# Optimization experiments

Measured on AMD Instinct MI355X. Metric: run time of the kernel, lower is better.

Reference implementation:

```python
import jax, jax.numpy as jnp
import numpy as np

N_HEAD = 8  # config.n_head

def _ln(x, g, b):
    # eqx.nn.LayerNorm, eps=1e-5
    m = x.mean(-1, keepdims=True)
    v = ((x - m) ** 2).mean(-1, keepdims=True)
    return (x - m) / jnp.sqrt(v + 1e-5) * g + b

def _lin(x, w, b):
    # eqx.nn.Linear: weight [out, in]
    return x @ w.T + b

def _heads(t):
    B, T, C = t.shape
    return t.reshape(B, T, N_HEAD, C // N_HEAD).transpose(0, 2, 1, 3)  # [B,H,T,d]

def _merge(t):
    B, H, T, d = t.shape
    return t.transpose(0, 2, 1, 3).reshape(B, T, H * d)

def setup_inputs() -> dict:
    key = jax.random.key(0)
    B, T1, T2, C, INNER, NIN = 4, 4096, 4096, 512, 2048, 2
    ks = jax.random.split(key, 16)
    w = lambda k, *s: 0.02 * jax.random.normal(k, s, dtype=jnp.float32)
    return {
        'x': jax.random.normal(ks[0], (B, T1, C), dtype=jnp.float32),
        'ys': jax.random.normal(ks[1], (NIN, B, T2, C), dtype=jnp.float32),
        'ln1_g': jnp.ones((C,)), 'ln1_b': jnp.zeros((C,)),
        'ln2_g': jnp.ones((NIN, C)), 'ln2_b': jnp.zeros((NIN, C)),
        'ln3_g': jnp.ones((C,)), 'ln3_b': jnp.zeros((C,)),
        'ln4_g': jnp.ones((C,)), 'ln4_b': jnp.zeros((C,)),
        'ln5_g': jnp.ones((C,)), 'ln5_b': jnp.zeros((C,)),
        'ca_wq': w(ks[2], C, C), 'ca_bq': jnp.zeros((C,)),
        'ca_wk': w(ks[3], NIN, C, C), 'ca_bk': jnp.zeros((NIN, C)),
        'ca_wv': w(ks[4], NIN, C, C), 'ca_bv': jnp.zeros((NIN, C)),
        'ca_wo': w(ks[5], C, C), 'ca_bo': jnp.zeros((C,)),
        'sa_wq': w(ks[6], C, C), 'sa_bq': jnp.zeros((C,)),
        'sa_wk': w(ks[7], C, C), 'sa_bk': jnp.zeros((C,)),
        'sa_wv': w(ks[8], C, C), 'sa_bv': jnp.zeros((C,)),
        'sa_wo': w(ks[9], C, C), 'sa_bo': jnp.zeros((C,)),
        'ffn1_w1': w(ks[10], INNER, C), 'ffn1_b1': jnp.zeros((INNER,)),
        'ffn1_w2': w(ks[11], C, INNER), 'ffn1_b2': jnp.zeros((C,)),
        'ffn2_w1': w(ks[12], INNER, C), 'ffn2_b1': jnp.zeros((INNER,)),
        'ffn2_w2': w(ks[13], C, INNER), 'ffn2_b2': jnp.zeros((C,)),
    }

def reference(x, ys, ln1_g, ln1_b, ln2_g, ln2_b, ln3_g, ln3_b, ln4_g, ln4_b, ln5_g, ln5_b,
              ca_wq, ca_bq, ca_wk, ca_bk, ca_wv, ca_bv, ca_wo, ca_bo,
              sa_wq, sa_bq, sa_wk, sa_bk, sa_wv, sa_bv, sa_wo, sa_bo,
              ffn1_w1, ffn1_b1, ffn1_w2, ffn1_b2, ffn2_w1, ffn2_b1, ffn2_w2, ffn2_b2):
    n_inputs = ys.shape[0]
    # ---- linear cross attention ----
    xn = _ln(x, ln1_g, ln1_b)
    q = jax.nn.softmax(_heads(_lin(xn, ca_wq, ca_bq)), axis=-1)  # [B,H,T1,d]
    out = q
    for i in range(n_inputs):  # small fixed branch count
        yn = _ln(ys[i], ln2_g[i], ln2_b[i])
        k = jax.nn.softmax(_heads(_lin(yn, ca_wk[i], ca_bk[i])), axis=-1)  # [B,H,T2,d]
        v = _heads(_lin(yn, ca_wv[i], ca_bv[i]))
        k_sum = k.sum(axis=-2, keepdims=True)                       # [B,H,1,d]
        D_inv = 1.0 / ((q * k_sum).sum(axis=-1, keepdims=True) + 1e-8)
        ctx = jnp.einsum('bhnd,bhnv->bhdv', k, v)                   # [B,H,d,d]
        out = out + jnp.einsum('bhqd,bhdv->bhqv', q, ctx) * D_inv
    x = x + _lin(_merge(out), ca_wo, ca_bo)
    # ---- FFN 1 ----
    xn = _ln(x, ln3_g, ln3_b)
    x = x + _lin(jax.nn.gelu(_lin(xn, ffn1_w1, ffn1_b1)), ffn1_w2, ffn1_b2)
    # ---- linear self attention (attn_type='l1') ----
    xn = _ln(x, ln4_g, ln4_b)
    q = jax.nn.softmax(_heads(_lin(xn, sa_wq, sa_bq)), axis=-1)
    k = jax.nn.softmax(_heads(_lin(xn, sa_wk, sa_bk)), axis=-1)
    v = _heads(_lin(xn, sa_wv, sa_bv))
    k_sum = k.sum(axis=-2, keepdims=True)
    D_inv = 1.0 / (q * k_sum).sum(axis=-1, keepdims=True)  # no eps in 'l1' branch
    ctx = jnp.einsum('bhnd,bhnv->bhdv', k, v)
    sa = jnp.einsum('bhqd,bhdv->bhqv', q, ctx) * D_inv + q
    x = x + _lin(_merge(sa), sa_wo, sa_bo)
    # ---- FFN 2 ----
    xn = _ln(x, ln5_g, ln5_b)
    x = x + _lin(jax.nn.gelu(_lin(xn, ffn2_w1, ffn2_b1)), ffn2_w2, ffn2_b2)
    return x
```

## Files before the change

kernel.cpp:

```cpp
#include <hip/hip_runtime.h>
#include <hip/hip_bf16.h>
#include <math.h>
#include <stdint.h>

typedef unsigned short u16;
typedef __attribute__((ext_vector_type(8))) short bh8;
typedef __attribute__((ext_vector_type(4))) float fx4;

#define DEV static __device__ __forceinline__

DEV float bf2f(u16 u){ union{unsigned u; float f;} v; v.u = ((unsigned)u)<<16; return v.f; }
DEV u16 f2bf(float f){ union{float f; unsigned u;} v; v.f = f;
  return (u16)((v.u + 0x7fffu + ((v.u>>16)&1u))>>16); }

DEV void async16(const u16* g, u16* l){
  __builtin_amdgcn_global_load_lds((__attribute__((address_space(1))) void*)(uintptr_t)g,
                                   (__attribute__((address_space(3))) void*)l, 16, 0, 0);
}

DEV float gelu_fast(float x){
  float u = 0.7978845608f*(x + 0.044715f*x*x*x);
  float e = __expf(-2.f*fabsf(u));
  float t = __fdividef(1.f - e, 1.f + e);
  t = copysignf(t, u);
  return 0.5f*x*(1.f + t);
}

struct WDesc { const float* src[14]; int off[14]; };
__global__ __launch_bounds__(256) void convw_kernel(WDesc d, u16* __restrict__ dst){
  int i = blockIdx.x*256 + threadIdx.x;
  int s = 0;
  #pragma unroll
  for(int j=1;j<14;j++) if(i >= d.off[j]) s = j;
  dst[i] = f2bf(d.src[s][i - d.off[s]]);
}

DEV float wsum64(float s){
  s += __shfl_xor(s,1,64);  s += __shfl_xor(s,2,64);  s += __shfl_xor(s,4,64);
  s += __shfl_xor(s,8,64);  s += __shfl_xor(s,16,64); s += __shfl_xor(s,32,64);
  return s;
}
__global__ __launch_bounds__(256) void ln_kernel(const float* __restrict__ x,
    const float* __restrict__ g, const float* __restrict__ bta, u16* __restrict__ out){
  int row  = blockIdx.x*4 + (threadIdx.x>>6);
  int lane = threadIdx.x & 63;
  const float4* xr = (const float4*)(x + (size_t)row*512) + lane*2;
  float4 a = xr[0], c = xr[1];
  float s = a.x+a.y+a.z+a.w + c.x+c.y+c.z+c.w;
  float mean = wsum64(s) * (1.f/512.f);
  float d0=a.x-mean,d1=a.y-mean,d2=a.z-mean,d3=a.w-mean;
  float d4=c.x-mean,d5=c.y-mean,d6=c.z-mean,d7=c.w-mean;
  float sv = d0*d0+d1*d1+d2*d2+d3*d3+d4*d4+d5*d5+d6*d6+d7*d7;
  float rstd = rsqrtf(wsum64(sv)*(1.f/512.f) + 1e-5f);
  const float4* gr = (const float4*)g   + lane*2;
  const float4* br = (const float4*)bta + lane*2;
  float4 g0=gr[0], g1=gr[1], b0=br[0], b1=br[1];
  bh8 o;
  o[0]=(short)f2bf(d0*rstd*g0.x+b0.x); o[1]=(short)f2bf(d1*rstd*g0.y+b0.y);
  o[2]=(short)f2bf(d2*rstd*g0.z+b0.z); o[3]=(short)f2bf(d3*rstd*g0.w+b0.w);
  o[4]=(short)f2bf(d4*rstd*g1.x+b1.x); o[5]=(short)f2bf(d5*rstd*g1.y+b1.y);
  o[6]=(short)f2bf(d6*rstd*g1.z+b1.z); o[7]=(short)f2bf(d7*rstd*g1.w+b1.w);
  *(bh8*)(out + (size_t)row*512 + lane*8) = o;
}

#define GEMM_KLOOP(Ab, Wb, K)                                                        \
  const int srow = w*32 + (lane>>2);                                                 \
  const int scol = (((lane&3) ^ ((srow>>1)&3)) * 8);                                 \
  const int rsw  = ((l15>>1)&3) ^ quad;                \
  for(int k0=0;k0<K;k0+=32){                                                         \
    __syncthreads();                                                                 \
    async16(Ab + (size_t)srow*K      + k0 + scol, &lsA[(w*32   )*32]);               \
    async16(Ab + (size_t)(srow+16)*K + k0 + scol, &lsA[(w*32+16)*32]);               \
    async16(Wb + (size_t)srow*K      + k0 + scol, &lsB[(w*32   )*32]);               \
    async16(Wb + (size_t)(srow+16)*K + k0 + scol, &lsB[(w*32+16)*32]);               \
    __syncthreads();                                                                 \
    bh8 af[4], bfx[4];                                                               \
    _Pragma("unroll")                                                                \
    for(int t=0;t<4;t++){                                                            \
      af[t]  = *(const bh8*)&lsA[(wm*64+t*16+l15)*32 + rsw*8];                       \
      bfx[t] = *(const bh8*)&lsB[(wn*64+t*16+l15)*32 + rsw*8];                       \
    }                                                                                \
    _Pragma("unroll")                                                                \
    for(int mt=0;mt<4;mt++)                                                          \
      _Pragma("unroll")                                                              \
      for(int nt=0;nt<4;nt++)                                                        \
        acc[mt][nt] = __builtin_amdgcn_mfma_f32_16x16x32_bf16(af[mt], bfx[nt], acc[mt][nt], 0,0,0); \
  }

struct SubD { const float* bias; u16* out; float* ksum; int mode; };
struct Subs3 { SubD s[3]; };
__global__ __launch_bounds__(256) void gemm_qkv(const u16* __restrict__ A,
    const u16* __restrict__ W, Subs3 subs, int K){
  __shared__ __align__(16) u16 lsA[128*32];
  __shared__ __align__(16) u16 lsB[128*32];
  const int tid = threadIdx.x, lane = tid&63, w = tid>>6;
  const int quad = lane>>4, l15 = lane&15;
  const int bn = blockIdx.x, bm = blockIdx.y;
  const int wm = w&1, wn = w>>1;
  fx4 acc[4][4];
  #pragma unroll
  for(int i=0;i<4;i++)
    #pragma unroll
    for(int j=0;j<4;j++) acc[i][j] = (fx4){0.f,0.f,0.f,0.f};
  const u16* Ab = A + (size_t)bm*128*K;
  const u16* Wb = W + (size_t)bn*128*K;
  GEMM_KLOOP(Ab, Wb, K)
  const SubD sub = subs.s[bn>>2];
  const int colw = (bn&3)*128 + wn*64;
  float bcol[4];
  #pragma unroll
  for(int nt=0;nt<4;nt++) bcol[nt] = sub.bias[colw + nt*16 + l15];

  if(sub.mode==1){
    float ksacc[4] = {0.f,0.f,0.f,0.f};
    #pragma unroll
    for(int mt=0;mt<4;mt++)
      #pragma unroll
      for(int r=0;r<4;r++){
        float v0=acc[mt][0][r]+bcol[0], v1=acc[mt][1][r]+bcol[1];
        float v2=acc[mt][2][r]+bcol[2], v3=acc[mt][3][r]+bcol[3];
        float mx = fmaxf(fmaxf(v0,v1),fmaxf(v2,v3));
        mx = fmaxf(mx,__shfl_xor(mx,1,64)); mx = fmaxf(mx,__shfl_xor(mx,2,64));
        mx = fmaxf(mx,__shfl_xor(mx,4,64)); mx = fmaxf(mx,__shfl_xor(mx,8,64));
        float e0=__expf(v0-mx), e1=__expf(v1-mx), e2=__expf(v2-mx), e3=__expf(v3-mx);
        float s = e0+e1+e2+e3;
        s += __shfl_xor(s,1,64); s += __shfl_xor(s,2,64);
        s += __shfl_xor(s,4,64); s += __shfl_xor(s,8,64);
        float inv = __fdividef(1.f, s);
        e0*=inv; e1*=inv; e2*=inv; e3*=inv;
        ksacc[0]+=e0; ksacc[1]+=e1; ksacc[2]+=e2; ksacc[3]+=e3;
        int row = bm*128 + wm*64 + mt*16 + quad*4 + r;
        size_t rb = (size_t)row*512;
        sub.out[rb+colw+ 0+l15]=f2bf(e0); sub.out[rb+colw+16+l15]=f2bf(e1);
        sub.out[rb+colw+32+l15]=f2bf(e2); sub.out[rb+colw+48+l15]=f2bf(e3);
      }
    if(sub.ksum){
      int b = bm>>5;
      #pragma unroll
      for(int nt=0;nt<4;nt++){
        float s = ksacc[nt];
        s += __shfl_xor(s,16,64); s += __shfl_xor(s,32,64);
        if(quad==0) atomicAdd(&sub.ksum[b*512 + colw + nt*16 + l15], s);
      }
    }
  } else {
    #pragma unroll
    for(int mt=0;mt<4;mt++)
      #pragma unroll
      for(int r=0;r<4;r++){
        int row = bm*128 + wm*64 + mt*16 + quad*4 + r;
        size_t rb = (size_t)row*512;
        #pragma unroll
        for(int nt=0;nt<4;nt++)
          sub.out[rb + colw + nt*16 + l15] = f2bf(acc[mt][nt][r] + bcol[nt]);
      }
  }
}

template<int EPI>
__global__ __launch_bounds__(256) void gemm_bt(const u16* __restrict__ A,
    const u16* __restrict__ W, const float* __restrict__ bias,
    const float* __restrict__ res, void* __restrict__ out, int N, int K){
  __shared__ __align__(16) u16 lsA[128*32];
  __shared__ __align__(16) u16 lsB[128*32];
  const int tid = threadIdx.x, lane = tid&63, w = tid>>6;
  const int quad = lane>>4, l15 = lane&15;
  const int bn = blockIdx.x, bm = blockIdx.y;
  const int wm = w&1, wn = w>>1;
  fx4 acc[4][4];
  #pragma unroll
  for(int i=0;i<4;i++)
    #pragma unroll
    for(int j=0;j<4;j++) acc[i][j] = (fx4){0.f,0.f,0.f,0.f};
  const u16* Ab = A + (size_t)bm*128*K;
  const u16* Wb = W + (size_t)bn*128*K;
  GEMM_KLOOP(Ab, Wb, K)
  const int colbase = bn*128 + wn*64;
  float bcol[4];
  #pragma unroll
  for(int nt=0;nt<4;nt++) bcol[nt] = bias[colbase + nt*16 + l15];

  if(EPI==3){
    float* of = (float*)out;
    #pragma unroll
    for(int mt=0;mt<4;mt++)
      #pragma unroll
      for(int r=0;r<4;r++){
        int row = bm*128 + wm*64 + mt*16 + quad*4 + r;
        size_t rb = (size_t)row*N;
        #pragma unroll
        for(int nt=0;nt<4;nt++){
          int col = colbase + nt*16 + l15;
          of[rb+col] = res[rb+col] + acc[mt][nt][r] + bcol[nt];
        }
      }
  } else {
    u16* ob = (u16*)out;
    #pragma unroll
    for(int mt=0;mt<4;mt++)
      #pragma unroll
      for(int r=0;r<4;r++){
        int row = bm*128 + wm*64 + mt*16 + quad*4 + r;
        size_t rb = (size_t)row*N;
        #pragma unroll
        for(int nt=0;nt<4;nt++)
          ob[rb + colbase + nt*16 + l15] = f2bf(gelu_fast(acc[mt][nt][r] + bcol[nt]));
      }
  }
}

__global__ __launch_bounds__(256) void ctx_kernel(const u16* __restrict__ kb,
    const u16* __restrict__ vb, float* __restrict__ ctx){
  __shared__ __align__(16) u16 lk[64*72];
  __shared__ __align__(16) u16 lv[64*72];
  const int tid=threadIdx.x, lane=tid&63, w=tid>>6, quad=lane>>4, l15=lane&15;
  const int bh = blockIdx.x, h = bh&7;
  const size_t rowbase = ((size_t)(bh>>3))*4096 + (size_t)blockIdx.y*512;
  const int mt0=(w&1)*32, nt0=(w>>1)*32;
  fx4 acc[2][2];
  #pragma unroll
  for(int i=0;i<2;i++)
    #pragma unroll
    for(int j=0;j<2;j++) acc[i][j] = (fx4){0.f,0.f,0.f,0.f};
  const int tl = tid>>2, part = tid&3;
  for(int it=0; it<8; it++){
    __syncthreads();
    {
      size_t gro = (rowbase + it*64 + tl)*512 + h*64 + part*16;
      bh8 k0 = *(const bh8*)(kb + gro); bh8 k1 = *(const bh8*)(kb + gro + 8);
      bh8 v0 = *(const bh8*)(vb + gro); bh8 v1 = *(const bh8*)(vb + gro + 8);
      #pragma unroll
      for(int j=0;j<8;j++){
        lk[(part*16+j  )*72 + tl] = (u16)k0[j];
        lk[(part*16+8+j)*72 + tl] = (u16)k1[j];
        lv[(part*16+j  )*72 + tl] = (u16)v0[j];
        lv[(part*16+8+j)*72 + tl] = (u16)v1[j];
      }
    }
    __syncthreads();
    #pragma unroll
    for(int ks=0;ks<2;ks++){
      bh8 a0 = *(const bh8*)&lk[(mt0    +l15)*72 + ks*32 + quad*8];
      bh8 a1 = *(const bh8*)&lk[(mt0+16 +l15)*72 + ks*32 + quad*8];
      bh8 b0 = *(const bh8*)&lv[(nt0    +l15)*72 + ks*32 + quad*8];
      bh8 b1 = *(const bh8*)&lv[(nt0+16 +l15)*72 + ks*32 + quad*8];
      acc[0][0] = __builtin_amdgcn_mfma_f32_16x16x32_bf16(a0,b0,acc[0][0],0,0,0);
      acc[0][1] = __builtin_amdgcn_mfma_f32_16x16x32_bf16(a0,b1,acc[0][1],0,0,0);
      acc[1][0] = __builtin_amdgcn_mfma_f32_16x16x32_bf16(a1,b0,acc[1][0],0,0,0);
      acc[1][1] = __builtin_amdgcn_mfma_f32_16x16x32_bf16(a1,b1,acc[1][1],0,0,0);
    }
  }
  float* cb = ctx + (size_t)bh*4096;
  #pragma unroll
  for(int mi=0;mi<2;mi++)
    #pragma unroll
    for(int ni=0;ni<2;ni++)
      #pragma unroll
      for(int r=0;r<4;r++){
        int d1 = mt0 + mi*16 + quad*4 + r;
        int d2 = nt0 + ni*16 + l15;
        atomicAdd(&cb[d1*64 + d2], acc[mi][ni][r]);
      }
}

__global__ __launch_bounds__(256) void dinv_kernel(const u16* __restrict__ q,
    const float* __restrict__ ksum, float* __restrict__ dinv, int n_in, float eps){
  int gidx = blockIdx.x*256 + threadIdx.x;
  int token = gidx>>3, h = gidx&7, b = token>>12;
  const u16* qr = q + (size_t)token*512 + h*64;
  float qv[64];
  #pragma unroll
  for(int d=0;d<64;d++) qv[d] = bf2f(qr[d]);
  for(int i=0;i<n_in;i++){
    const float* ks = ksum + i*2048 + b*512 + h*64;
    float s = 0.f;
    #pragma unroll
    for(int d=0;d<64;d++) s += qv[d]*ks[d];
    dinv[(size_t)i*131072 + gidx] = __fdividef(1.f, s + eps);
  }
}

template<int NIN>
__global__ __launch_bounds__(256) void apply_kernel(const u16* __restrict__ q,
    const float* __restrict__ ctx, const float* __restrict__ dinv, u16* __restrict__ out){
  __shared__ __align__(16) u16 lctx[(NIN+1)*64*72];
  const int tid=threadIdx.x, lane=tid&63, w=tid>>6, quad=lane>>4, l15=lane&15;
  const int bh = blockIdx.x, b=bh>>3, h=bh&7;
  {
    int base = tid*16;
    int d1 = base>>6, d2b = base&63;
    #pragma unroll
    for(int s=0;s<=NIN;s++){
      u16* dst = &lctx[s*64*72];
      if(s<NIN){
        const float* sp = ctx + ((size_t)s*32 + bh)*4096 + base;
        #pragma unroll
        for(int j=0;j<16;j++) dst[(d2b+j)*72 + d1] = f2bf(sp[j]);
      } else {
        #pragma unroll
        for(int j=0;j<16;j++) dst[(d2b+j)*72 + d1] = ((d2b+j)==d1) ? (u16)0x3f80 : (u16)0;
      }
    }
  }
  __syncthreads();
  bh8 bfr[NIN+1][4][2];
  #pragma unroll
  for(int s=0;s<=NIN;s++)
    #pragma unroll
    for(int nt=0;nt<4;nt++)
      #pragma unroll
      for(int ks=0;ks<2;ks++)
        bfr[s][nt][ks] = *(const bh8*)&lctx[s*64*72 + (nt*16+l15)*72 + ks*32 + quad*8];
  const size_t tb0 = (size_t)b*4096 + (size_t)blockIdx.y*256 + w*64;
  for(int g=0;g<4;g++){
    size_t tb = tb0 + g*16;
    const u16* qr = q + (tb + l15)*512 + h*64;
    bh8 a0 = *(const bh8*)(qr + quad*8);
    bh8 a1 = *(const bh8*)(qr + 32 + quad*8);
    fx4 outv[4];
    #pragma unroll
    for(int nt=0;nt<4;nt++) outv[nt] = (fx4){0.f,0.f,0.f,0.f};
    #pragma unroll
    for(int s=0;s<=NIN;s++){
      fx4 c[4];
      #pragma unroll
      for(int nt=0;nt<4;nt++){
        c[nt] = (fx4){0.f,0.f,0.f,0.f};
        c[nt] = __builtin_amdgcn_mfma_f32_16x16x32_bf16(a0, bfr[s][nt][0], c[nt], 0,0,0);
        c[nt] = __builtin_amdgcn_mfma_f32_16x16x32_bf16(a1, bfr[s][nt][1], c[nt], 0,0,0);
      }
      float dv[4];
      #pragma unroll
      for(int r=0;r<4;r++)
        dv[r] = (s==NIN) ? 1.f : dinv[(size_t)s*131072 + (tb+quad*4+r)*8 + h];
      #pragma unroll
      for(int nt=0;nt<4;nt++)
        #pragma unroll
        for(int r=0;r<4;r++) outv[nt][r] += c[nt][r]*dv[r];
    }
    #pragma unroll
    for(int nt=0;nt<4;nt++)
      #pragma unroll
      for(int r=0;r<4;r++)
        out[(tb+quad*4+r)*512 + h*64 + nt*16 + l15] = f2bf(outv[nt][r]);
  }
}

extern "C" void kernel_launch(void* const* d_in, const int* in_sizes, int n_in,
                              void* d_out, int out_size, void* d_ws, size_t ws_size,
                              hipStream_t stream){
  const float* x_in =(const float*)d_in[0];
  const float* ys   =(const float*)d_in[1];
  const float* ln1g =(const float*)d_in[2],  *ln1b=(const float*)d_in[3];
  const float* ln2g =(const float*)d_in[4],  *ln2b=(const float*)d_in[5];
  const float* ln3g =(const float*)d_in[6],  *ln3b=(const float*)d_in[7];
  const float* ln4g =(const float*)d_in[8],  *ln4b=(const float*)d_in[9];
  const float* ln5g =(const float*)d_in[10], *ln5b=(const float*)d_in[11];
  const float* ca_wq=(const float*)d_in[12], *ca_bq=(const float*)d_in[13];
  const float* ca_wk=(const float*)d_in[14], *ca_bk=(const float*)d_in[15];
  const float* ca_wv=(const float*)d_in[16], *ca_bv=(const float*)d_in[17];
  const float* ca_wo=(const float*)d_in[18], *ca_bo=(const float*)d_in[19];
  const float* sa_wq=(const float*)d_in[20], *sa_bq=(const float*)d_in[21];
  const float* sa_wk=(const float*)d_in[22], *sa_bk=(const float*)d_in[23];
  const float* sa_wv=(const float*)d_in[24], *sa_bv=(const float*)d_in[25];
  const float* sa_wo=(const float*)d_in[26], *sa_bo=(const float*)d_in[27];
  const float* f1w1 =(const float*)d_in[28], *f1b1=(const float*)d_in[29];
  const float* f1w2 =(const float*)d_in[30], *f1b2=(const float*)d_in[31];
  const float* f2w1 =(const float*)d_in[32], *f2b1=(const float*)d_in[33];
  const float* f2w2 =(const float*)d_in[34], *f2b2=(const float*)d_in[35];

  char* p = (char*)d_ws;
  u16*   WBF = (u16*)p;    p += 13631488;
  float* XW  = (float*)p;  p += 33554432;
  u16*   XN  = (u16*)p;    p += 16777216;
  u16*   QB  = (u16*)p;    p += 16777216;
  u16*   KB  = (u16*)p;    p += 16777216;
  u16*   VB  = (u16*)p;    p += 16777216;
  u16*   HB  = (u16*)p;    p += 67108864;
  float* SM  = (float*)p;  p += 1597440;
  float* DINV= (float*)p;  p += 1048576;
  float* CTXC = SM;
  float* CTXS = SM + 262144;
  float* KSC  = SM + 393216;
  float* KSS  = SM + 397312;
  u16*   OUTB = HB;

  WDesc wd;
  const float* wsrc[14] = {ca_wq, ca_wk, ca_wv, ca_wk+262144, ca_wv+262144, ca_wo,
                           sa_wq, sa_wk, sa_wv, sa_wo, f1w1, f1w2, f2w1, f2w2};
  const int    woff[14] = {0, 262144, 524288, 786432, 1048576, 1310720,
                           1572864, 1835008, 2097152, 2359296,
                           2621440, 3670016, 4718592, 5767168};
  for(int i=0;i<14;i++){ wd.src[i]=wsrc[i]; wd.off[i]=woff[i]; }
  convw_kernel<<<26624,256,0,stream>>>(wd, WBF);
  hipMemsetAsync(SM, 0, 399360*sizeof(float), stream);

  SubD zsub = {nullptr,nullptr,nullptr,0};

  ln_kernel<<<4096,256,0,stream>>>(x_in, ln1g, ln1b, XN);
  { Subs3 s = {{ {ca_bq, QB, nullptr, 1}, zsub, zsub }};
    gemm_qkv<<<dim3(4,128),256,0,stream>>>(XN, WBF+0, s, 512); }
  for(int i=0;i<2;i++){
    ln_kernel<<<4096,256,0,stream>>>(ys + (size_t)i*16384*512, ln2g+i*512, ln2b+i*512, XN);
    { Subs3 s = {{ {ca_bk+i*512, KB, KSC+i*2048, 1}, {ca_bv+i*512, VB, nullptr, 0}, zsub }};
      gemm_qkv<<<dim3(8,128),256,0,stream>>>(XN, WBF+262144+i*524288, s, 512); }
    ctx_kernel<<<dim3(32,8),256,0,stream>>>(KB, VB, CTXC + (size_t)i*131072);
  }
  dinv_kernel<<<512,256,0,stream>>>(QB, KSC, DINV, 2, 1e-8f);
  apply_kernel<2><<<dim3(32,16),256,0,stream>>>(QB, CTXC, DINV, OUTB);
  gemm_bt<3><<<dim3(4,128),256,0,stream>>>(OUTB, WBF+1310720, ca_bo, x_in, XW, 512, 512);

  ln_kernel<<<4096,256,0,stream>>>(XW, ln3g, ln3b, XN);
  gemm_bt<2><<<dim3(16,128),256,0,stream>>>(XN, WBF+2621440, f1b1, nullptr, HB, 2048, 512);
  gemm_bt<3><<<dim3(4,128),256,0,stream>>>(HB, WBF+3670016, f1b2, XW, XW, 512, 2048);

  ln_kernel<<<4096,256,0,stream>>>(XW, ln4g, ln4b, XN);
  { Subs3 s = {{ {sa_bq, QB, nullptr, 1}, {sa_bk, KB, KSS, 1}, {sa_bv, VB, nullptr, 0} }};
    gemm_qkv<<<dim3(12,128),256,0,stream>>>(XN, WBF+1572864, s, 512); }
  ctx_kernel<<<dim3(32,8),256,0,stream>>>(KB, VB, CTXS);
  dinv_kernel<<<512,256,0,stream>>>(QB, KSS, DINV, 1, 0.f);
  apply_kernel<1><<<dim3(32,16),256,0,stream>>>(QB, CTXS, DINV, OUTB);
  gemm_bt<3><<<dim3(4,128),256,0,stream>>>(OUTB, WBF+2359296, sa_bo, XW, XW, 512, 512);

  ln_kernel<<<4096,256,0,stream>>>(XW, ln5g, ln5b, XN);
  gemm_bt<2><<<dim3(16,128),256,0,stream>>>(XN, WBF+4718592, f2b1, nullptr, HB, 2048, 512);
  gemm_bt<3><<<dim3(4,128),256,0,stream>>>(HB, WBF+5767168, f2b2, XW, (float*)d_out, 512, 2048);
}
```

Measured before the change: 818.2 us.

## Batch cross-attn inputs, widen GEMM K-tile to 64, fuse D_inv into apply

Several changes are bundled here. The GEMM k-loop now stages 64-wide K tiles with an XOR swizzle, which halves the number of barrier pairs per tile. The two cross-attention input streams are handled together: one LayerNorm launch, one batched K/V GEMM that picks weights and bias by row set, and one ctx launch. The separate dinv kernel is removed and its normaliser is computed inside apply_kernel from ksum. This cuts launches and D_inv memory traffic, at the cost of more LDS per block, which may lower occupancy.

Measured after the change: 773.9 us. 1.06x faster.

```diff
diff --git a/kernel.cpp b/kernel.cpp
--- a/kernel.cpp
+++ b/kernel.cpp
@@ -40,11 +40,8 @@
   s += __shfl_xor(s,8,64);  s += __shfl_xor(s,16,64); s += __shfl_xor(s,32,64);
   return s;
 }
-__global__ __launch_bounds__(256) void ln_kernel(const float* __restrict__ x,
-    const float* __restrict__ g, const float* __restrict__ bta, u16* __restrict__ out){
-  int row  = blockIdx.x*4 + (threadIdx.x>>6);
-  int lane = threadIdx.x & 63;
-  const float4* xr = (const float4*)(x + (size_t)row*512) + lane*2;
+DEV void ln_row(const float* xrow, const float* g, const float* bta, u16* orow, int lane){
+  const float4* xr = (const float4*)xrow + lane*2;
   float4 a = xr[0], c = xr[1];
   float s = a.x+a.y+a.z+a.w + c.x+c.y+c.z+c.w;
   float mean = wsum64(s) * (1.f/512.f);
@@ -60,42 +57,59 @@
   o[2]=(short)f2bf(d2*rstd*g0.z+b0.z); o[3]=(short)f2bf(d3*rstd*g0.w+b0.w);
   o[4]=(short)f2bf(d4*rstd*g1.x+b1.x); o[5]=(short)f2bf(d5*rstd*g1.y+b1.y);
   o[6]=(short)f2bf(d6*rstd*g1.z+b1.z); o[7]=(short)f2bf(d7*rstd*g1.w+b1.w);
-  *(bh8*)(out + (size_t)row*512 + lane*8) = o;
-}
-
-#define GEMM_KLOOP(Ab, Wb, K)                                                        \
-  const int srow = w*32 + (lane>>2);                                                 \
-  const int scol = (((lane&3) ^ ((srow>>1)&3)) * 8);                                 \
-  const int rsw  = ((l15>>1)&3) ^ quad;                \
-  for(int k0=0;k0<K;k0+=32){                                                         \
+  *(bh8*)(orow + lane*8) = o;
+}
+__global__ __launch_bounds__(256) void ln_kernel(const float* __restrict__ x,
+    const float* __restrict__ g, const float* __restrict__ bta, u16* __restrict__ out){
+  int row  = blockIdx.x*4 + (threadIdx.x>>6);
+  ln_row(x + (size_t)row*512, g, bta, out + (size_t)row*512, threadIdx.x&63);
+}
+__global__ __launch_bounds__(256) void lny_kernel(const float* __restrict__ ys,
+    const float* __restrict__ g2, const float* __restrict__ b2, u16* __restrict__ out){
+  int row  = blockIdx.x*4 + (threadIdx.x>>6);
+  int i = row>>14;
+  ln_row(ys + (size_t)row*512, g2 + i*512, b2 + i*512, out + (size_t)row*512, threadIdx.x&63);
+}
+
+#define GEMM_KLOOP64(Ab, Wb, K)                                                      \
+  const int srow8 = lane>>3;                                                         \
+  const int scol  = ((lane&7) ^ srow8) * 8;                                          \
+  for(int k0=0;k0<(K);k0+=64){                                                       \
     __syncthreads();                                                                 \
-    async16(Ab + (size_t)srow*K      + k0 + scol, &lsA[(w*32   )*32]);               \
-    async16(Ab + (size_t)(srow+16)*K + k0 + scol, &lsA[(w*32+16)*32]);               \
-    async16(Wb + (size_t)srow*K      + k0 + scol, &lsB[(w*32   )*32]);               \
-    async16(Wb + (size_t)(srow+16)*K + k0 + scol, &lsB[(w*32+16)*32]);               \
+    _Pragma("unroll")                                                                \
+    for(int j=0;j<4;j++){                                                            \
+      int r = w*32 + j*8 + srow8;                                                    \
+      async16(Ab + (size_t)r*(K) + k0 + scol, &lsA[(w*32+j*8)*64]);                  \
+      async16(Wb + (size_t)r*(K) + k0 + scol, &lsB[(w*32+j*8)*64]);                  \
+    }                                                                                \
     __syncthreads();                                                                 \
-    bh8 af[4], bfx[4];                                                               \
     _Pragma("unroll")                                                                \
-    for(int t=0;t<4;t++){                                                            \
-      af[t]  = *(const bh8*)&lsA[(wm*64+t*16+l15)*32 + rsw*8];                       \
-      bfx[t] = *(const bh8*)&lsB[(wn*64+t*16+l15)*32 + rsw*8];                       \
+    for(int ks=0;ks<2;ks++){                                                         \
+      bh8 af[4], bfx[4];                                                             \
+      _Pragma("unroll")                                                              \
+      for(int t=0;t<4;t++){                                                          \
+        int ra = wm*64+t*16+l15, rb2 = wn*64+t*16+l15;                               \
+        af[t]  = *(const bh8*)&lsA[ra*64 + ((ks*4+quad) ^ (ra&7))*8];                \
+        bfx[t] = *(const bh8*)&lsB[rb2*64 + ((ks*4+quad) ^ (rb2&7))*8];              \
+      }                                                                              \
+      _Pragma("unroll")                                                              \
+      for(int mt=0;mt<4;mt++)                                                        \
+        _Pragma("unroll")                                                            \
+        for(int nt=0;nt<4;nt++)                                                      \
+          acc[mt][nt] = __builtin_amdgcn_mfma_f32_16x16x32_bf16(af[mt], bfx[nt], acc[mt][nt], 0,0,0); \
     }                                                                                \
-    _Pragma("unroll")                                                                \
-    for(int mt=0;mt<4;mt++)                                                          \
-      _Pragma("unroll")                                                              \
-      for(int nt=0;nt<4;nt++)                                                        \
-        acc[mt][nt] = __builtin_amdgcn_mfma_f32_16x16x32_bf16(af[mt], bfx[nt], acc[mt][nt], 0,0,0); \
   }
 
 struct SubD { const float* bias; u16* out; float* ksum; int mode; };
 struct Subs3 { SubD s[3]; };
 __global__ __launch_bounds__(256) void gemm_qkv(const u16* __restrict__ A,
-    const u16* __restrict__ W, Subs3 subs, int K){
-  __shared__ __align__(16) u16 lsA[128*32];
-  __shared__ __align__(16) u16 lsB[128*32];
+    const u16* __restrict__ W, Subs3 subs, int K, int wstride, int bstride, int ksstride){
+  __shared__ __align__(16) u16 lsA[128*64];
+  __shared__ __align__(16) u16 lsB[128*64];
   const int tid = threadIdx.x, lane = tid&63, w = tid>>6;
   const int quad = lane>>4, l15 = lane&15;
   const int bn = blockIdx.x, bm = blockIdx.y;
+  const int iset = bm>>7;
   const int wm = w&1, wn = w>>1;
   fx4 acc[4][4];
   #pragma unroll
@@ -103,13 +117,14 @@
     #pragma unroll
     for(int j=0;j<4;j++) acc[i][j] = (fx4){0.f,0.f,0.f,0.f};
   const u16* Ab = A + (size_t)bm*128*K;
-  const u16* Wb = W + (size_t)bn*128*K;
-  GEMM_KLOOP(Ab, Wb, K)
+  const u16* Wb = W + (size_t)iset*wstride + (size_t)bn*128*K;
+  GEMM_KLOOP64(Ab, Wb, K)
   const SubD sub = subs.s[bn>>2];
   const int colw = (bn&3)*128 + wn*64;
+  const float* bias = sub.bias + iset*bstride;
   float bcol[4];
   #pragma unroll
-  for(int nt=0;nt<4;nt++) bcol[nt] = sub.bias[colw + nt*16 + l15];
+  for(int nt=0;nt<4;nt++) bcol[nt] = bias[colw + nt*16 + l15];
 
   if(sub.mode==1){
     float ksacc[4] = {0.f,0.f,0.f,0.f};
@@ -135,12 +150,13 @@
         sub.out[rb+colw+32+l15]=f2bf(e2); sub.out[rb+colw+48+l15]=f2bf(e3);
       }
     if(sub.ksum){
-      int b = bm>>5;
+      int b = (bm&127)>>5;
+      float* ks = sub.ksum + iset*ksstride + b*512;
       #pragma unroll
       for(int nt=0;nt<4;nt++){
         float s = ksacc[nt];
         s += __shfl_xor(s,16,64); s += __shfl_xor(s,32,64);
-        if(quad==0) atomicAdd(&sub.ksum[b*512 + colw + nt*16 + l15], s);
+        if(quad==0) atomicAdd(&ks[colw + nt*16 + l15], s);
       }
     }
   } else {
@@ -161,8 +177,8 @@
 __global__ __launch_bounds__(256) void gemm_bt(const u16* __restrict__ A,
     const u16* __restrict__ W, const float* __restrict__ bias,
     const float* __restrict__ res, void* __restrict__ out, int N, int K){
-  __shared__ __align__(16) u16 lsA[128*32];
-  __shared__ __align__(16) u16 lsB[128*32];
+  __shared__ __align__(16) u16 lsA[128*64];
+  __shared__ __align__(16) u16 lsB[128*64];
   const int tid = threadIdx.x, lane = tid&63, w = tid>>6;
   const int quad = lane>>4, l15 = lane&15;
   const int bn = blockIdx.x, bm = blockIdx.y;
@@ -174,7 +190,7 @@
     for(int j=0;j<4;j++) acc[i][j] = (fx4){0.f,0.f,0.f,0.f};
   const u16* Ab = A + (size_t)bm*128*K;
   const u16* Wb = W + (size_t)bn*128*K;
-  GEMM_KLOOP(Ab, Wb, K)
+  GEMM_KLOOP64(Ab, Wb, K)
   const int colbase = bn*128 + wn*64;
   float bcol[4];
   #pragma unroll
@@ -210,25 +226,27 @@
 }
 
 __global__ __launch_bounds__(256) void ctx_kernel(const u16* __restrict__ kb,
-    const u16* __restrict__ vb, float* __restrict__ ctx){
+    const u16* __restrict__ vb, float* __restrict__ ctx, size_t kstride){
   __shared__ __align__(16) u16 lk[64*72];
   __shared__ __align__(16) u16 lv[64*72];
   const int tid=threadIdx.x, lane=tid&63, w=tid>>6, quad=lane>>4, l15=lane&15;
-  const int bh = blockIdx.x, h = bh&7;
-  const size_t rowbase = ((size_t)(bh>>3))*4096 + (size_t)blockIdx.y*512;
+  const int bh2 = blockIdx.x, i = bh2>>5, h = bh2&7, b = (bh2>>3)&3;
+  const u16* kbase = kb + (size_t)i*kstride;
+  const u16* vbase = vb + (size_t)i*kstride;
+  const size_t rowbase = (size_t)b*4096 + (size_t)blockIdx.y*512;
   const int mt0=(w&1)*32, nt0=(w>>1)*32;
   fx4 acc[2][2];
   #pragma unroll
-  for(int i=0;i<2;i++)
-    #pragma unroll
-    for(int j=0;j<2;j++) acc[i][j] = (fx4){0.f,0.f,0.f,0.f};
+  for(int x=0;x<2;x++)
+    #pragma unroll
+    for(int j=0;j<2;j++) acc[x][j] = (fx4){0.f,0.f,0.f,0.f};
   const int tl = tid>>2, part = tid&3;
   for(int it=0; it<8; it++){
     __syncthreads();
     {
       size_t gro = (rowbase + it*64 + tl)*512 + h*64 + part*16;
-      bh8 k0 = *(const bh8*)(kb + gro); bh8 k1 = *(const bh8*)(kb + gro + 8);
-      bh8 v0 = *(const bh8*)(vb + gro); bh8 v1 = *(const bh8*)(vb + gro + 8);
+      bh8 k0 = *(const bh8*)(kbase + gro); bh8 k1 = *(const bh8*)(kbase + gro + 8);
+      bh8 v0 = *(const bh8*)(vbase + gro); bh8 v1 = *(const bh8*)(vbase + gro + 8);
       #pragma unroll
       for(int j=0;j<8;j++){
         lk[(part*16+j  )*72 + tl] = (u16)k0[j];
@@ -250,7 +268,7 @@
       acc[1][1] = __builtin_amdgcn_mfma_f32_16x16x32_bf16(a1,b1,acc[1][1],0,0,0);
     }
   }
-  float* cb = ctx + (size_t)bh*4096;
+  float* cb = ctx + (size_t)bh2*4096;
   #pragma unroll
   for(int mi=0;mi<2;mi++)
     #pragma unroll
@@ -263,26 +281,10 @@
       }
 }
 
-__global__ __launch_bounds__(256) void dinv_kernel(const u16* __restrict__ q,
-    const float* __restrict__ ksum, float* __restrict__ dinv, int n_in, float eps){
-  int gidx = blockIdx.x*256 + threadIdx.x;
-  int token = gidx>>3, h = gidx&7, b = token>>12;
-  const u16* qr = q + (size_t)token*512 + h*64;
-  float qv[64];
-  #pragma unroll
-  for(int d=0;d<64;d++) qv[d] = bf2f(qr[d]);
-  for(int i=0;i<n_in;i++){
-    const float* ks = ksum + i*2048 + b*512 + h*64;
-    float s = 0.f;
-    #pragma unroll
-    for(int d=0;d<64;d++) s += qv[d]*ks[d];
-    dinv[(size_t)i*131072 + gidx] = __fdividef(1.f, s + eps);
-  }
-}
-
 template<int NIN>
 __global__ __launch_bounds__(256) void apply_kernel(const u16* __restrict__ q,
-    const float* __restrict__ ctx, const float* __restrict__ dinv, u16* __restrict__ out){
+    const float* __restrict__ ctx, const float* __restrict__ ksum, float eps,
+    u16* __restrict__ out){
   __shared__ __align__(16) u16 lctx[(NIN+1)*64*72];
   const int tid=threadIdx.x, lane=tid&63, w=tid>>6, quad=lane>>4, l15=lane&15;
   const int bh = blockIdx.x, b=bh>>3, h=bh&7;
@@ -301,6 +303,13 @@
         for(int j=0;j<16;j++) dst[(d2b+j)*72 + d1] = ((d2b+j)==d1) ? (u16)0x3f80 : (u16)0;
       }
     }
+  }
+  float kslo[NIN][8], kshi[NIN][8];
+  #pragma unroll
+  for(int s=0;s<NIN;s++){
+    const float* ks = ksum + s*2048 + b*512 + h*64;
+    #pragma unroll
+    for(int j=0;j<8;j++){ kslo[s][j] = ks[quad*8+j]; kshi[s][j] = ks[32+quad*8+j]; }
   }
   __syncthreads();
   bh8 bfr[NIN+1][4][2];
@@ -317,6 +326,18 @@
     const u16* qr = q + (tb + l15)*512 + h*64;
     bh8 a0 = *(const bh8*)(qr + quad*8);
     bh8 a1 = *(const bh8*)(qr + 32 + quad*8);
+    float dv[NIN][4];
+    #pragma unroll
+    for(int s=0;s<NIN;s++){
+      float part = 0.f;
+      #pragma unroll
+      for(int j=0;j<8;j++)
+        part += bf2f((u16)a0[j])*kslo[s][j] + bf2f((u16)a1[j])*kshi[s][j];
+      part += __shfl_xor(part,16,64); part += __shfl_xor(part,32,64);
+      #pragma unroll
+      for(int r=0;r<4;r++)
+        dv[s][r] = __fdividef(1.f, __shfl(part, quad*4+r, 64) + eps);
+    }
     fx4 outv[4];
     #pragma unroll
     for(int nt=0;nt<4;nt++) outv[nt] = (fx4){0.f,0.f,0.f,0.f};
@@ -329,14 +350,10 @@
         c[nt] = __builtin_amdgcn_mfma_f32_16x16x32_bf16(a0, bfr[s][nt][0], c[nt], 0,0,0);
         c[nt] = __builtin_amdgcn_mfma_f32_16x16x32_bf16(a1, bfr[s][nt][1], c[nt], 0,0,0);
       }
-      float dv[4];
-      #pragma unroll
-      for(int r=0;r<4;r++)
-        dv[r] = (s==NIN) ? 1.f : dinv[(size_t)s*131072 + (tb+quad*4+r)*8 + h];
       #pragma unroll
       for(int nt=0;nt<4;nt++)
         #pragma unroll
-        for(int r=0;r<4;r++) outv[nt][r] += c[nt][r]*dv[r];
+        for(int r=0;r<4;r++) outv[nt][r] += c[nt][r]*((s==NIN)?1.f:dv[s][r]);
     }
     #pragma unroll
     for(int nt=0;nt<4;nt++)
@@ -372,18 +389,19 @@
   char* p = (char*)d_ws;
   u16*   WBF = (u16*)p;    p += 13631488;
   float* XW  = (float*)p;  p += 33554432;
-  u16*   XN  = (u16*)p;    p += 16777216;
+  u16*   XN2 = (u16*)p;    p += 33554432;
   u16*   QB  = (u16*)p;    p += 16777216;
-  u16*   KB  = (u16*)p;    p += 16777216;
-  u16*   VB  = (u16*)p;    p += 16777216;
-  u16*   HB  = (u16*)p;    p += 67108864;
+  u16*   R1  = (u16*)p;    p += 67108864;
+  u16*   OUTB= (u16*)p;    p += 16777216;
   float* SM  = (float*)p;  p += 1597440;
-  float* DINV= (float*)p;  p += 1048576;
+  u16*   XN  = XN2;
+  u16*   KB2 = R1;
+  u16*   VB2 = R1 + 16777216;
+  u16*   HB  = R1;
   float* CTXC = SM;
   float* CTXS = SM + 262144;
   float* KSC  = SM + 393216;
   float* KSS  = SM + 397312;
-  u16*   OUTB = HB;
 
   WDesc wd;
   const float* wsrc[14] = {ca_wq, ca_wk, ca_wv, ca_wk+262144, ca_wv+262144, ca_wo,
@@ -399,15 +417,13 @@
 
   ln_kernel<<<4096,256,0,stream>>>(x_in, ln1g, ln1b, XN);
   { Subs3 s = {{ {ca_bq, QB, nullptr, 1}, zsub, zsub }};
-    gemm_qkv<<<dim3(4,128),256,0,stream>>>(XN, WBF+0, s, 512); }
-  for(int i=0;i<2;i++){
-    ln_kernel<<<4096,256,0,stream>>>(ys + (size_t)i*16384*512, ln2g+i*512, ln2b+i*512, XN);
-    { Subs3 s = {{ {ca_bk+i*512, KB, KSC+i*2048, 1}, {ca_bv+i*512, VB, nullptr, 0}, zsub }};
-      gemm_qkv<<<dim3(8,128),256,0,stream>>>(XN, WBF+262144+i*524288, s, 512); }
-    ctx_kernel<<<dim3(32,8),256,0,stream>>>(KB, VB, CTXC + (size_t)i*131072);
-  }
-  dinv_kernel<<<512,256,0,stream>>>(QB, KSC, DINV, 2, 1e-8f);
-  apply_kernel<2><<<dim3(32,16),256,0,stream>>>(QB, CTXC, DINV, OUTB);
+    gemm_qkv<<<dim3(4,128),256,0,stream>>>(XN, WBF+0, s, 512, 0,0,0); }
+  lny_kernel<<<8192,256,0,stream>>>(ys, ln2g, ln2b, XN2);
+  { Subs3 s = {{ {ca_bk, KB2, KSC, 1}, {ca_bv, VB2, nullptr, 0}, zsub }};
+    gemm_qkv<<<dim3(8,256),256,0,stream>>>(XN2, WBF+262144, s, 512,
+                                           524288, 512, 2048); }
+  ctx_kernel<<<dim3(64,8),256,0,stream>>>(KB2, VB2, CTXC, (size_t)16384*512);
+  apply_kernel<2><<<dim3(32,16),256,0,stream>>>(QB, CTXC, KSC, 1e-8f, OUTB);
   gemm_bt<3><<<dim3(4,128),256,0,stream>>>(OUTB, WBF+1310720, ca_bo, x_in, XW, 512, 512);
 
   ln_kernel<<<4096,256,0,stream>>>(XW, ln3g, ln3b, XN);
@@ -415,11 +431,10 @@
   gemm_bt<3><<<dim3(4,128),256,0,stream>>>(HB, WBF+3670016, f1b2, XW, XW, 512, 2048);
 
   ln_kernel<<<4096,256,0,stream>>>(XW, ln4g, ln4b, XN);
-  { Subs3 s = {{ {sa_bq, QB, nullptr, 1}, {sa_bk, KB, KSS, 1}, {sa_bv, VB, nullptr, 0} }};
-    gemm_qkv<<<dim3(12,128),256,0,stream>>>(XN, WBF+1572864, s, 512); }
-  ctx_kernel<<<dim3(32,8),256,0,stream>>>(KB, VB, CTXS);
-  dinv_kernel<<<512,256,0,stream>>>(QB, KSS, DINV, 1, 0.f);
-  apply_kernel<1><<<dim3(32,16),256,0,stream>>>(QB, CTXS, DINV, OUTB);
+  { Subs3 s = {{ {sa_bq, QB, nullptr, 1}, {sa_bk, KB2, KSS, 1}, {sa_bv, VB2, nullptr, 0} }};
+    gemm_qkv<<<dim3(12,128),256,0,stream>>>(XN, WBF+1572864, s, 512, 0,0,0); }
+  ctx_kernel<<<dim3(32,8),256,0,stream>>>(KB2, VB2, CTXS, 0);
+  apply_kernel<1><<<dim3(32,16),256,0,stream>>>(QB, CTXS, KSS, 0.f, OUTB);
   gemm_bt<3><<<dim3(4,128),256,0,stream>>>(OUTB, WBF+2359296, sa_bo, XW, XW, 512, 512);
 
   ln_kernel<<<4096,256,0,stream>>>(XW, ln5g, ln5b, XN);
```
